# Optimization experiments

Hardware: AMD Instinct MI355X
Metric: run time of the kernel (lower is better)

The kernel has to match this reference:

```python
import jax, jax.numpy as jnp
import numpy as np

N_EMBED = 1024
N_HEADS = 16
HEAD_SIZE = N_EMBED // N_HEADS


def setup_inputs() -> dict:
    key = jax.random.key(0)
    ks = jax.random.split(key, 9)
    d = N_EMBED
    s = 1.0 / np.sqrt(d)
    return {
        "x": jax.random.normal(ks[0], (2, 2048, d), dtype=jnp.float32),
        "Wq": jax.random.uniform(ks[1], (d, d), jnp.float32, -s, s),
        "bq": jax.random.uniform(ks[2], (d,), jnp.float32, -s, s),
        "Wk": jax.random.uniform(ks[3], (d, d), jnp.float32, -s, s),
        "bk": jax.random.uniform(ks[4], (d,), jnp.float32, -s, s),
        "Wv": jax.random.uniform(ks[5], (d, d), jnp.float32, -s, s),
        "bv": jax.random.uniform(ks[6], (d,), jnp.float32, -s, s),
        "Wo": jax.random.uniform(ks[7], (d, d), jnp.float32, -s, s),
        "bo": jax.random.uniform(ks[8], (d,), jnp.float32, -s, s),
    }


def reference(x, Wq, bq, Wk, bk, Wv, bv, Wo, bo):
    B, T, D = x.shape
    H, Hd = N_HEADS, HEAD_SIZE
    # projections (torch Linear: x @ W^T + b; here W stored already transposed)
    q = (x @ Wq + bq).reshape(B, T, H, Hd).transpose(0, 2, 1, 3)  # [B,H,T,Hd]
    k = (x @ Wk + bk).reshape(B, T, H, Hd).transpose(0, 2, 1, 3)
    v = (x @ Wv + bv).reshape(B, T, H, Hd).transpose(0, 2, 1, 3)
    scores = jnp.einsum("bhqd,bhkd->bhqk", q, k) * (Hd ** -0.5)  # [B,H,T,T]
    causal = jnp.tril(jnp.ones((T, T), dtype=bool))
    scores = jnp.where(causal[None, None], scores, -jnp.inf)
    probs = jax.nn.softmax(scores, axis=-1)
    out = jnp.einsum("bhqk,bhkd->bhqd", probs, v)  # [B,H,T,Hd]
    out = out.transpose(0, 2, 1, 3).reshape(B, T, D)
    return out @ Wo + bo
```

## Files before the change

kernel.cpp:

```cpp
#include <hip/hip_runtime.h>
#include <cstdint>
#include <cstddef>

typedef __bf16 bf16;
typedef __bf16 bf16x4 __attribute__((ext_vector_type(4)));
typedef __bf16 bf16x8 __attribute__((ext_vector_type(8)));
typedef float  f32x4  __attribute__((ext_vector_type(4)));
typedef float  f32x16 __attribute__((ext_vector_type(16)));

#define B_  2
#define T_  2048
#define D_  1024
#define H_  16
#define HD_ 64
#define M_  (B_ * T_)
#define NQB 32

#define GLOAD_LDS(gsrc, ldst) \
    __builtin_amdgcn_global_load_lds( \
        (const __attribute__((address_space(1))) void*)(gsrc), \
        (__attribute__((address_space(3))) void*)(ldst), 16, 0, 0)

__device__ __forceinline__ float exp2_fast(float x) {
    float r;
    asm("v_exp_f32 %0, %1" : "=v"(r) : "v"(x));
    return r;
}

#define MAX3(a, b, c) fmaxf(fmaxf((a), (b)), (c))

__device__ __forceinline__ void barrier_pin() {
    asm volatile("" ::: "memory");
    __builtin_amdgcn_s_barrier();
    asm volatile("" ::: "memory");
}

__global__ void prep_kernel(
    const float* __restrict__ x,  bf16* __restrict__ xb,
    const float* __restrict__ W0, bf16* __restrict__ T0,
    const float* __restrict__ W1, bf16* __restrict__ T1,
    const float* __restrict__ W2, bf16* __restrict__ T2,
    const float* __restrict__ W3, bf16* __restrict__ T3)
{
    if (blockIdx.z == 4) {
        const int linear = blockIdx.y * 32 + blockIdx.x;
        const int base = linear * 4096 + threadIdx.x * 4;
        #pragma unroll
        for (int u = 0; u < 4; ++u) {
            const int i = base + u * 1024;
            const float4 v = *reinterpret_cast<const float4*>(x + i);
            bf16x4 o = { (bf16)v.x, (bf16)v.y, (bf16)v.z, (bf16)v.w };
            *reinterpret_cast<bf16x4*>(xb + i) = o;
        }
        return;
    }
    __shared__ float tile[32][33];
    const float* W = blockIdx.z == 0 ? W0 : blockIdx.z == 1 ? W1 : blockIdx.z == 2 ? W2 : W3;
    bf16*       Wt = blockIdx.z == 0 ? T0 : blockIdx.z == 1 ? T1 : blockIdx.z == 2 ? T2 : T3;
    const int tx = threadIdx.x & 31, ty = threadIdx.x >> 5;
    const int bx = blockIdx.x * 32, by = blockIdx.y * 32;
    #pragma unroll
    for (int r = 0; r < 32; r += 8)
        tile[ty + r][tx] = W[(size_t)(by + ty + r) * D_ + bx + tx];
    __syncthreads();
    #pragma unroll
    for (int r = 0; r < 32; r += 8)
        Wt[(size_t)(bx + ty + r) * D_ + by + tx] = (bf16)tile[tx][ty + r];
}

__global__ __launch_bounds__(512, 2) void qkv256_kernel(
    const bf16* __restrict__ xb,
    const bf16* __restrict__ WqT, const float* __restrict__ bq, bf16* __restrict__ Qo,
    const bf16* __restrict__ WkT, const float* __restrict__ bk, bf16* __restrict__ Ko,
    const bf16* __restrict__ WvT, const float* __restrict__ bv, bf16* __restrict__ Vt)
{
    __shared__ bf16 As[2][2][128][64];
    __shared__ bf16 Bs[2][2][128][64];

    const int bid = blockIdx.x;
    const int swz = (bid & 7) * 24 + (bid >> 3);
    const int tid = threadIdx.x, wave = tid >> 6, lane = tid & 63;
    const int lr = lane & 15, lg = lane >> 4;
    const int wr = wave >> 2, wc = wave & 3;

    const bf16 *Aop, *Bop;
    const float *bias;
    bf16 *outp;
    float scale = 1.0f;
    int mbase, nbase, mode;
    if (swz < 128) {
        const int bm = swz >> 3, bn = swz & 7;
        mbase = bm * 256;
        nbase = (bn & 3) * 256;
        Aop = xb + (size_t)mbase * D_;
        if (bn < 4) { Bop = WqT + (size_t)nbase * D_; bias = bq; outp = Qo;
                      scale = 0.125f * 1.44269504f; }
        else        { Bop = WkT + (size_t)nbase * D_; bias = bk; outp = Ko; }
        mode = 0;
    } else {
        const int v = swz - 128, bm = v >> 4, bn = v & 15;
        mbase = bm * 256;
        nbase = bn * 256;
        Aop = WvT + (size_t)mbase * D_;
        Bop = xb  + (size_t)nbase * D_;
        bias = bv; outp = Vt; mode = 1;
    }

    const int r8   = lane >> 3;
    const int srcc = (lane & 7) ^ r8;
    auto stageA = [&](int c, int h, int kt) {
        #pragma unroll
        for (int l = 0; l < 2; ++l) {
            const int cr  = wave * 2 + l;
            const int loc = cr * 8 + r8;
            const int rho = h * 64 + (loc & 63) + ((loc >> 6) << 7);
            GLOAD_LDS(Aop + (size_t)rho * D_ + kt * 64 + srcc * 8, &As[c][h][cr * 8][0]);
        }
    };
    auto stageB = [&](int c, int h, int kt) {
        #pragma unroll
        for (int l = 0; l < 2; ++l) {
            const int cr  = wave * 2 + l;
            const int loc = cr * 8 + r8;
            const int rho = h * 32 + (loc & 31) + ((loc >> 5) << 6);
            GLOAD_LDS(Bop + (size_t)rho * D_ + kt * 64 + srcc * 8, &Bs[c][h][cr * 8][0]);
        }
    };

    f32x4 acc[8][4] = {};
    bf16x8 ar[4][2], b0r[2][2], b1r[2][2];

    auto LDA = [&](int c, int mh) {
        #pragma unroll
        for (int i = 0; i < 4; ++i)
            #pragma unroll
            for (int kk = 0; kk < 2; ++kk)
                ar[i][kk] = *reinterpret_cast<const bf16x8*>(
                    &As[c][mh][wr * 64 + i * 16 + lr][(((kk * 4 + lg)) ^ (lr & 7)) * 8]);
    };
    auto LDB = [&](int c, int nh, bf16x8 (&br)[2][2]) {
        #pragma unroll
        for (int j = 0; j < 2; ++j)
            #pragma unroll
            for (int kk = 0; kk < 2; ++kk)
                br[j][kk] = *reinterpret_cast<const bf16x8*>(
                    &Bs[c][nh][wc * 32 + j * 16 + lr][(((kk * 4 + lg)) ^ (lr & 7)) * 8]);
    };
    auto QUAD = [&](const bf16x8 (&br)[2][2], int mh, int nh) {
        __builtin_amdgcn_s_setprio(1);
        #pragma unroll
        for (int i = 0; i < 4; ++i)
            #pragma unroll
            for (int j = 0; j < 2; ++j)
                #pragma unroll
                for (int kk = 0; kk < 2; ++kk)
                    acc[mh * 4 + i][nh * 2 + j] = __builtin_amdgcn_mfma_f32_16x16x32_bf16(
                        ar[i][kk], br[j][kk], acc[mh * 4 + i][nh * 2 + j], 0, 0, 0);
        __builtin_amdgcn_s_setprio(0);
    };

    constexpr int NK = D_ / 64;
    stageA(0, 0, 0); stageB(0, 0, 0); stageA(0, 1, 0); stageB(0, 1, 0);
    stageA(1, 0, 1); stageB(1, 1, 1);
    asm volatile("s_waitcnt vmcnt(4)" ::: "memory");
    barrier_pin();

    #pragma unroll 1
    for (int t = 0; t < NK; ++t) {
        const int c = t & 1, cn = c ^ 1;
        const bool h1 = (t + 1 < NK), h2 = (t + 2 < NK);
        LDA(c, 0); LDB(c, 0, b0r);
        if (h1) stageA(cn, 1, t + 1);
        barrier_pin();
        QUAD(b0r, 0, 0);
        barrier_pin();
        LDB(c, 1, b1r);
        if (h1) stageB(cn, 0, t + 1);
        barrier_pin();
        QUAD(b1r, 0, 1);
        barrier_pin();
        LDA(c, 1);
        if (h2) stageA(c, 0, t + 2);
        barrier_pin();
        QUAD(b1r, 1, 1);
        barrier_pin();
        if (h2) stageB(c, 1, t + 2);
        asm volatile("s_waitcnt vmcnt(4)" ::: "memory");
        barrier_pin();
        QUAD(b0r, 1, 0);
        barrier_pin();
    }

    if (mode == 0) {
        #pragma unroll
        for (int i = 0; i < 8; ++i)
            #pragma unroll
            for (int j = 0; j < 4; ++j)
                #pragma unroll
                for (int r = 0; r < 4; ++r) {
                    const int m  = mbase + wr * 128 + i * 16 + lg * 4 + r;
                    const int nw = nbase + wc * 64 + j * 16 + lr;
                    const float val = (acc[i][j][r] + bias[nw]) * scale;
                    const int b = m >> 11, tt = m & (T_ - 1);
                    const int h = nw >> 6, hd = nw & 63;
                    outp[((size_t)((b * H_ + h) * T_ + tt)) * HD_ + hd] = (bf16)val;
                }
    } else {
        #pragma unroll
        for (int i = 0; i < 8; ++i)
            #pragma unroll
            for (int j = 0; j < 4; ++j)
                #pragma unroll
                for (int r = 0; r < 4; ++r) {
                    const int d = mbase + wr * 128 + i * 16 + lg * 4 + r;
                    const int n = nbase + wc * 64 + j * 16 + lr;
                    const int b = n >> 11, tt = n & (T_ - 1);
                    outp[((size_t)(b * D_ + d)) * T_ + tt] = (bf16)(acc[i][j][r] + bias[d]);
                }
    }
}

__global__ __launch_bounds__(256, 2) void gemm_out_kernel(
    const bf16* __restrict__ A, const bf16* __restrict__ WoT,
    const float* __restrict__ bo, float* __restrict__ Out)
{
    constexpr int K = D_;
    constexpr int NK = K / 64;
    __shared__ bf16 As[2][64][64];
    __shared__ bf16 Bs[2][128][64];

    const int bid = blockIdx.x;
    const int swz = (bid & 7) * 64 + (bid >> 3);
    const int m0 = (swz & 63) * 64, n0 = (swz >> 6) * 128;

    const int tid = threadIdx.x, wave = tid >> 6, lane = tid & 63;
    const int l5 = lane & 31, hi = lane >> 5;
    const int rseg = lane >> 3;
    const int srcc = (lane & 7) ^ rseg;

    auto stage = [&](int b, int k0) {
        #pragma unroll
        for (int cc = 0; cc < 2; ++cc) {
            const int seg = wave * 2 + cc;
            const int row = seg * 8 + rseg;
            GLOAD_LDS(A + (size_t)(m0 + row) * K + k0 + srcc * 8, &As[b][seg * 8][0]);
        }
        #pragma unroll
        for (int cc = 0; cc < 4; ++cc) {
            const int seg = wave * 4 + cc;
            const int row = seg * 8 + rseg;
            GLOAD_LDS(WoT + (size_t)(n0 + row) * K + k0 + srcc * 8, &Bs[b][seg * 8][0]);
        }
    };

    f32x16 acc[2] = {};
    stage(0, 0);
    __syncthreads();

    #pragma unroll 1
    for (int t = 0; t < NK; ++t) {
        const int cur = t & 1;
        if (t + 1 < NK) stage(cur ^ 1, (t + 1) * 64);

        bf16x8 af[2][4], bfr[4];
        #pragma unroll
        for (int mi = 0; mi < 2; ++mi)
            #pragma unroll
            for (int ks = 0; ks < 4; ++ks) {
                const int row = mi * 32 + l5;
                af[mi][ks] = *reinterpret_cast<const bf16x8*>(
                    &As[cur][row][((ks * 2 + hi) ^ (row & 7)) * 8]);
            }
        #pragma unroll
        for (int ks = 0; ks < 4; ++ks) {
            const int row = wave * 32 + l5;
            bfr[ks] = *reinterpret_cast<const bf16x8*>(
                &Bs[cur][row][((ks * 2 + hi) ^ (row & 7)) * 8]);
        }
        __builtin_amdgcn_s_setprio(1);
        #pragma unroll
        for (int mi = 0; mi < 2; ++mi)
            #pragma unroll
            for (int ks = 0; ks < 4; ++ks)
                acc[mi] = __builtin_amdgcn_mfma_f32_32x32x16_bf16(
                    af[mi][ks], bfr[ks], acc[mi], 0, 0, 0);
        __builtin_amdgcn_s_setprio(0);
        __syncthreads();
    }

    #pragma unroll
    for (int mi = 0; mi < 2; ++mi)
        #pragma unroll
        for (int q = 0; q < 16; ++q) {
            const int m = m0 + mi * 32 + (q & 3) + 8 * (q >> 2) + 4 * hi;
            const int n = n0 + wave * 32 + l5;
            Out[(size_t)m * D_ + n] = acc[mi][q] + bo[n];
        }
}

__global__ __launch_bounds__(256) void attn_kernel(
    const bf16* __restrict__ Q, const bf16* __restrict__ K,
    const bf16* __restrict__ Vt, bf16* __restrict__ Out)
{
    const int bid = blockIdx.x;
    const int xcd = bid & 7, j = bid >> 3;
    const int bh  = xcd * 4 + (j >> 4);
    const int pr  = j & 15;

    const int tid = threadIdx.x, wave = tid >> 6, lane = tid & 63;
    const int lr = lane & 15, lg = lane >> 4;
    const size_t kbase = (size_t)bh * T_ * HD_;
    const size_t vbase = (size_t)bh * HD_ * T_;

    __shared__ bf16 Ks[2][64][64];
    __shared__ bf16 Vs[2][64][64];
    __shared__ bf16 Ps[4][16][72];

    auto stage = [&](int sb, int kt) {
        const int kv0 = kt * 64;
        const int rseg = lane >> 3;
        const int srcw = (lane & 7) ^ rseg;
        #pragma unroll
        for (int cc = 0; cc < 2; ++cc) {
            const int seg = wave * 2 + cc;
            const int row = seg * 8 + rseg;
            GLOAD_LDS(K  + kbase + (size_t)(kv0 + row) * HD_ + srcw * 8, &Ks[sb][seg * 8][0]);
            GLOAD_LDS(Vt + vbase + (size_t)row * T_ + kv0 + srcw * 8,    &Vs[sb][seg * 8][0]);
        }
    };
    auto kfrag = [&](int sb, int row, int chunk) {
        return *reinterpret_cast<const bf16x8*>(&Ks[sb][row][(chunk ^ (row & 7)) * 8]);
    };
    auto vfrag = [&](int sb, int row, int chunk) {
        return *reinterpret_cast<const bf16x8*>(&Vs[sb][row][(chunk ^ (row & 7)) * 8]);
    };

    #pragma unroll 1
    for (int half = 0; half < 2; ++half) {
        const int qb = half == 0 ? pr : (NQB - 1 - pr);
        const int q0 = qb * 64;
        const int nt = qb + 1;
        const int qw = wave * 16;

        bf16x8 qf[2];
        {
            const bf16* qrow = Q + kbase + (size_t)(q0 + qw + lr) * HD_;
            qf[0] = *reinterpret_cast<const bf16x8*>(qrow + lg * 8);
            qf[1] = *reinterpret_cast<const bf16x8*>(qrow + 32 + lg * 8);
        }

        float m_s = -1e30f, l_s = 0.f;
        f32x4 o_acc[4] = {};

        stage(0, 0);
        __syncthreads();

        #pragma unroll 1
        for (int t = 0; t < nt; ++t) {
            const int cur = t & 1;
            if (t + 1 < nt) stage(cur ^ 1, t + 1);

            const int kv0 = t * 64;
            f32x4 s[4] = {};
            __builtin_amdgcn_s_setprio(1);
            #pragma unroll
            for (int n16 = 0; n16 < 4; ++n16)
                #pragma unroll
                for (int kk = 0; kk < 2; ++kk)
                    s[n16] = __builtin_amdgcn_mfma_f32_16x16x32_bf16(
                        kfrag(cur, n16 * 16 + lr, kk * 4 + lg), qf[kk], s[n16], 0, 0, 0);
            __builtin_amdgcn_s_setprio(0);
            if (t == qb) {
                #pragma unroll
                for (int n16 = 0; n16 < 4; ++n16)
                    #pragma unroll
                    for (int r = 0; r < 4; ++r)
                        if (kv0 + n16 * 16 + lg * 4 + r > q0 + qw + lr)
                            s[n16][r] = -1e30f;
            }
            const float t0 = MAX3(s[0][0], s[0][1], s[0][2]);
            const float t1 = MAX3(s[0][3], s[1][0], s[1][1]);
            const float t2 = MAX3(s[1][2], s[1][3], s[2][0]);
            const float t3 = MAX3(s[2][1], s[2][2], s[2][3]);
            const float t4 = MAX3(s[3][0], s[3][1], s[3][2]);
            const float mx = fmaxf(MAX3(t0, t1, t2), MAX3(t3, t4, s[3][3]));
            if (__any(mx > m_s + 11.5416f)) {
                float rmx = fmaxf(mx, __shfl_xor(mx, 16));
                rmx = fmaxf(rmx, __shfl_xor(rmx, 32));
                const float mnew  = fmaxf(m_s, rmx);
                const float alpha = exp2_fast(m_s - mnew);
                #pragma unroll
                for (int r = 0; r < 4; ++r) {
                    const float a = __shfl(alpha, lg * 4 + r);
                    #pragma unroll
                    for (int nd = 0; nd < 4; ++nd) o_acc[nd][r] *= a;
                }
                l_s *= alpha;
                m_s = mnew;
            }
            float ls0 = 0.f, ls1 = 0.f, ls2 = 0.f, ls3 = 0.f;
            #pragma unroll
            for (int n16 = 0; n16 < 4; ++n16) {
                bf16x4 pw;
                const float p0 = exp2_fast(s[n16][0] - m_s);
                const float p1 = exp2_fast(s[n16][1] - m_s);
                const float p2 = exp2_fast(s[n16][2] - m_s);
                const float p3 = exp2_fast(s[n16][3] - m_s);
                ls0 += p0; ls1 += p1; ls2 += p2; ls3 += p3;
                pw[0] = (bf16)p0; pw[1] = (bf16)p1; pw[2] = (bf16)p2; pw[3] = (bf16)p3;
                *reinterpret_cast<bf16x4*>(&Ps[wave][lr][n16 * 16 + lg * 4]) = pw;
            }
            l_s += (ls0 + ls1) + (ls2 + ls3);
            __builtin_amdgcn_s_setprio(1);
            #pragma unroll
            for (int ks = 0; ks < 2; ++ks) {
                const bf16x8 pa = *reinterpret_cast<const bf16x8*>(&Ps[wave][lr][ks * 32 + lg * 8]);
                #pragma unroll
                for (int nd = 0; nd < 4; ++nd)
                    o_acc[nd] = __builtin_amdgcn_mfma_f32_16x16x32_bf16(
                        pa, vfrag(cur, nd * 16 + lr, ks * 4 + lg), o_acc[nd], 0, 0, 0);
            }
            __builtin_amdgcn_s_setprio(0);
            __syncthreads();
        }

        l_s += __shfl_xor(l_s, 16);
        l_s += __shfl_xor(l_s, 32);

        const int b = bh >> 4, h = bh & 15;
        const float linv = 1.0f / l_s;
        #pragma unroll
        for (int r = 0; r < 4; ++r) {
            const float li = __shfl(linv, lg * 4 + r);
            const int q = q0 + qw + lg * 4 + r;
            #pragma unroll
            for (int nd = 0; nd < 4; ++nd) {
                const int d = nd * 16 + lr;
                Out[((size_t)(b * T_ + q)) * D_ + h * HD_ + d] = (bf16)(o_acc[nd][r] * li);
            }
        }
    }
}

extern "C" void kernel_launch(void* const* d_in, const int* in_sizes, int n_in,
                              void* d_out, int out_size, void* d_ws, size_t ws_size,
                              hipStream_t stream) {
    const float* x  = (const float*)d_in[0];
    const float* Wq = (const float*)d_in[1];
    const float* bq = (const float*)d_in[2];
    const float* Wk = (const float*)d_in[3];
    const float* bk = (const float*)d_in[4];
    const float* Wv = (const float*)d_in[5];
    const float* bv = (const float*)d_in[6];
    const float* Wo = (const float*)d_in[7];
    const float* bo = (const float*)d_in[8];
    float* out = (float*)d_out;

    char* ws = (char*)d_ws;
    bf16* xb   = (bf16*)(ws);
    bf16* WqT  = (bf16*)(ws + ( 8u << 20));
    bf16* WkT  = (bf16*)(ws + (10u << 20));
    bf16* WvT  = (bf16*)(ws + (12u << 20));
    bf16* WoT  = (bf16*)(ws + (14u << 20));
    bf16* Qb   = (bf16*)(ws + (16u << 20));
    bf16* Kb   = (bf16*)(ws + (24u << 20));
    bf16* Vtb  = (bf16*)(ws + (32u << 20));
    bf16* attn = (bf16*)(ws + (40u << 20));

    prep_kernel<<<dim3(32, 32, 5), 256, 0, stream>>>(
        x, xb, Wq, WqT, Wk, WkT, Wv, WvT, Wo, WoT);

    qkv256_kernel<<<192, 512, 0, stream>>>(xb, WqT, bq, Qb, WkT, bk, Kb, WvT, bv, Vtb);

    attn_kernel<<<512, 256, 0, stream>>>(Qb, Kb, Vtb, attn);

    gemm_out_kernel<<<512, 256, 0, stream>>>(attn, WoT, bo, out);
}
```

Measured before the change: 106.3 us.

## Software-pipeline QK^T one tile ahead with triple-buffered K/V in LDS

Moves to a three-stage K/V LDS ring and computes the next tile's QK^T scores before the current tile's softmax and PV MMAs. The aim is to overlap MFMA score work with the exp/max VALU work and to hide global-to-LDS load latency two tiles ahead. In exchange, LDS use and register pressure go up (two sets of score accumulators), which may lower occupancy. The loop's barrier now sits at the top of each iteration.

Measured after the change: 111.3 us. 4.7% more time.

```diff
diff --git a/kernel.cpp b/kernel.cpp
--- a/kernel.cpp
+++ b/kernel.cpp
@@ -312,8 +312,8 @@
     const size_t kbase = (size_t)bh * T_ * HD_;
     const size_t vbase = (size_t)bh * HD_ * T_;
 
-    __shared__ bf16 Ks[2][64][64];
-    __shared__ bf16 Vs[2][64][64];
+    __shared__ bf16 Ks[3][64][64];
+    __shared__ bf16 Vs[3][64][64];
     __shared__ bf16 Ps[4][16][72];
 
     auto stage = [&](int sb, int kt) {
@@ -351,39 +351,57 @@
 
         float m_s = -1e30f, l_s = 0.f;
         f32x4 o_acc[4] = {};
+        f32x4 sp[4], sc[4];
 
         stage(0, 0);
         __syncthreads();
+        #pragma unroll
+        for (int n16 = 0; n16 < 4; ++n16) sp[n16] = f32x4{};
+        __builtin_amdgcn_s_setprio(1);
+        #pragma unroll
+        for (int n16 = 0; n16 < 4; ++n16)
+            #pragma unroll
+            for (int kk = 0; kk < 2; ++kk)
+                sp[n16] = __builtin_amdgcn_mfma_f32_16x16x32_bf16(
+                    kfrag(0, n16 * 16 + lr, kk * 4 + lg), qf[kk], sp[n16], 0, 0, 0);
+        __builtin_amdgcn_s_setprio(0);
+        if (nt > 1) stage(1, 1);
 
         #pragma unroll 1
         for (int t = 0; t < nt; ++t) {
-            const int cur = t & 1;
-            if (t + 1 < nt) stage(cur ^ 1, t + 1);
+            __syncthreads();
+            if (t + 2 < nt) stage((t + 2) % 3, t + 2);
+
+            #pragma unroll
+            for (int n16 = 0; n16 < 4; ++n16) sc[n16] = f32x4{};
+            if (t + 1 < nt) {
+                const int nb = (t + 1) % 3;
+                __builtin_amdgcn_s_setprio(1);
+                #pragma unroll
+                for (int n16 = 0; n16 < 4; ++n16)
+                    #pragma unroll
+                    for (int kk = 0; kk < 2; ++kk)
+                        sc[n16] = __builtin_amdgcn_mfma_f32_16x16x32_bf16(
+                            kfrag(nb, n16 * 16 + lr, kk * 4 + lg), qf[kk], sc[n16], 0, 0, 0);
+                __builtin_amdgcn_s_setprio(0);
+            }
 
             const int kv0 = t * 64;
-            f32x4 s[4] = {};
-            __builtin_amdgcn_s_setprio(1);
-            #pragma unroll
-            for (int n16 = 0; n16 < 4; ++n16)
-                #pragma unroll
-                for (int kk = 0; kk < 2; ++kk)
-                    s[n16] = __builtin_amdgcn_mfma_f32_16x16x32_bf16(
-                        kfrag(cur, n16 * 16 + lr, kk * 4 + lg), qf[kk], s[n16], 0, 0, 0);
-            __builtin_amdgcn_s_setprio(0);
+            const int cb = t % 3;
             if (t == qb) {
                 #pragma unroll
                 for (int n16 = 0; n16 < 4; ++n16)
                     #pragma unroll
                     for (int r = 0; r < 4; ++r)
                         if (kv0 + n16 * 16 + lg * 4 + r > q0 + qw + lr)
-                            s[n16][r] = -1e30f;
-            }
-            const float t0 = MAX3(s[0][0], s[0][1], s[0][2]);
-            const float t1 = MAX3(s[0][3], s[1][0], s[1][1]);
-            const float t2 = MAX3(s[1][2], s[1][3], s[2][0]);
-            const float t3 = MAX3(s[2][1], s[2][2], s[2][3]);
-            const float t4 = MAX3(s[3][0], s[3][1], s[3][2]);
-            const float mx = fmaxf(MAX3(t0, t1, t2), MAX3(t3, t4, s[3][3]));
+                            sp[n16][r] = -1e30f;
+            }
+            const float t0 = MAX3(sp[0][0], sp[0][1], sp[0][2]);
+            const float t1 = MAX3(sp[0][3], sp[1][0], sp[1][1]);
+            const float t2 = MAX3(sp[1][2], sp[1][3], sp[2][0]);
+            const float t3 = MAX3(sp[2][1], sp[2][2], sp[2][3]);
+            const float t4 = MAX3(sp[3][0], sp[3][1], sp[3][2]);
+            const float mx = fmaxf(MAX3(t0, t1, t2), MAX3(t3, t4, sp[3][3]));
             if (__any(mx > m_s + 11.5416f)) {
                 float rmx = fmaxf(mx, __shfl_xor(mx, 16));
                 rmx = fmaxf(rmx, __shfl_xor(rmx, 32));
@@ -402,10 +420,10 @@
             #pragma unroll
             for (int n16 = 0; n16 < 4; ++n16) {
                 bf16x4 pw;
-                const float p0 = exp2_fast(s[n16][0] - m_s);
-                const float p1 = exp2_fast(s[n16][1] - m_s);
-                const float p2 = exp2_fast(s[n16][2] - m_s);
-                const float p3 = exp2_fast(s[n16][3] - m_s);
+                const float p0 = exp2_fast(sp[n16][0] - m_s);
+                const float p1 = exp2_fast(sp[n16][1] - m_s);
+                const float p2 = exp2_fast(sp[n16][2] - m_s);
+                const float p3 = exp2_fast(sp[n16][3] - m_s);
                 ls0 += p0; ls1 += p1; ls2 += p2; ls3 += p3;
                 pw[0] = (bf16)p0; pw[1] = (bf16)p1; pw[2] = (bf16)p2; pw[3] = (bf16)p3;
                 *reinterpret_cast<bf16x4*>(&Ps[wave][lr][n16 * 16 + lg * 4]) = pw;
@@ -418,11 +436,12 @@
                 #pragma unroll
                 for (int nd = 0; nd < 4; ++nd)
                     o_acc[nd] = __builtin_amdgcn_mfma_f32_16x16x32_bf16(
-                        pa, vfrag(cur, nd * 16 + lr, ks * 4 + lg), o_acc[nd], 0, 0, 0);
+                        pa, vfrag(cb, nd * 16 + lr, ks * 4 + lg), o_acc[nd], 0, 0, 0);
             }
             __builtin_amdgcn_s_setprio(0);
-            __syncthreads();
-        }
+            sp[0] = sc[0]; sp[1] = sc[1]; sp[2] = sc[2]; sp[3] = sc[3];
+        }
+        __syncthreads();
 
         l_s += __shfl_xor(l_s, 16);
         l_s += __shfl_xor(l_s, 32);
```
